# Optimization experiments

Hardware: AMD Instinct MI355X
Metric: run time of the kernel (lower is better)

The kernel has to match this reference:

```python
import jax, jax.numpy as jnp
import numpy as np

D = 160          # SDF grid resolution (D1=D2=D3=D)
LEVEL = 0.0      # marching_cubes(-sdf, level=-0) == level 0 on s = -sdf
N_SMOOTH = 2
LAMBD = 1.0


def _extract_mesh_np():
    """Host-side isosurface extraction (mirrors the module's CPU round-trip).
    Uses marching tetrahedra (6-tet cube decomposition) in place of skimage's
    lewiner marching cubes; topo_correct (undefined in source) is identity.
    Returns (verts [V,3] f32 in normalized coords, faces [F,3] i32, edges [E,2] i32).
    """
    xs = np.arange(D, dtype=np.float32)
    X, Y, Z = np.meshgrid(xs, xs, xs, indexing='ij')
    ctr = (D - 1) / 2.0
    sdf = np.sqrt((X - ctr) ** 2 + (Y - ctr) ** 2 + (Z - ctr) ** 2) - 0.35 * D
    sdf = sdf + 3.0 * np.sin(0.20 * X) * np.sin(0.17 * Y) * np.sin(0.23 * Z)
    s = (-sdf).astype(np.float32)  # extract level-0 isosurface of -sdf
    sflat = s.ravel()
    Ng = D ** 3

    corner_off = [(0, 0, 0), (1, 0, 0), (1, 1, 0), (0, 1, 0),
                  (0, 0, 1), (1, 0, 1), (1, 1, 1), (0, 1, 1)]
    b = np.arange(D - 1)
    BX, BY, BZ = np.meshgrid(b, b, b, indexing='ij')
    BX, BY, BZ = BX.ravel(), BY.ravel(), BZ.ravel()
    gid8 = [((BX + dx) * D + (BY + dy)) * D + (BZ + dz) for dx, dy, dz in corner_off]
    val8 = [sflat[g] for g in gid8]

    TETS = [(0, 5, 1, 6), (0, 1, 2, 6), (0, 2, 3, 6),
            (0, 3, 7, 6), (0, 7, 4, 6), (0, 4, 5, 6)]
    TE = [(0, 1), (0, 2), (0, 3), (1, 2), (1, 3), (2, 3)]  # tet edges
    CASE_TRIS = {1: [(0, 1, 2)], 14: [(0, 1, 2)],
                 2: [(0, 3, 4)], 13: [(0, 3, 4)],
                 4: [(1, 3, 5)], 11: [(1, 3, 5)],
                 8: [(2, 4, 5)], 7: [(2, 4, 5)],
                 3: [(1, 3, 4), (1, 4, 2)], 12: [(1, 3, 4), (1, 4, 2)],
                 5: [(0, 3, 5), (0, 5, 2)], 10: [(0, 3, 5), (0, 5, 2)],
                 6: [(0, 4, 5), (0, 5, 1)], 9: [(0, 4, 5), (0, 5, 1)]}
    bitw = np.array([1, 2, 4, 8])

    tri_keys = []
    for tet in TETS:
        tv = np.stack([val8[c] for c in tet], 1)  # [Nc,4] corner values
        tg = np.stack([gid8[c] for c in tet], 1)  # [Nc,4] corner grid ids
        case = (tv < LEVEL).astype(np.int64) @ bitw
        for c, tris in CASE_TRIS.items():
            sel = np.nonzero(case == c)[0]
            if sel.size == 0:
                continue
            g = tg[sel]
            for tri in tris:
                cols = []
                for e in tri:
                    i, j = TE[e]
                    lo = np.minimum(g[:, i], g[:, j])
                    hi = np.maximum(g[:, i], g[:, j])
                    cols.append(lo * Ng + hi)  # canonical grid-edge key
                tri_keys.append(np.stack(cols, 1))
    tris = np.concatenate(tri_keys, 0)  # [F,3] edge keys
    uk, inv = np.unique(tris, return_inverse=True)
    faces = inv.reshape(-1, 3).astype(np.int32)
    ga = uk // Ng
    gb = uk % Ng
    pa = np.stack(np.unravel_index(ga, (D, D, D)), 1).astype(np.float32)
    pb = np.stack(np.unravel_index(gb, (D, D, D)), 1).astype(np.float32)
    sa = sflat[ga]
    sb = sflat[gb]
    t = ((LEVEL - sa) / (sb - sa)).astype(np.float32)
    verts = pa + t[:, None] * (pb - pa)
    verts = (2.0 * verts - np.float32(D)) / np.float32(D)  # (2v-[D1,D2,D3])/D
    e = np.concatenate([faces[:, [0, 1]], faces[:, [1, 2]], faces[:, [2, 0]]], 0)
    e = np.unique(np.sort(e, 1), axis=0).astype(np.int32)
    return verts.astype(np.float32), faces, e


def setup_inputs() -> dict:
    verts, faces, edges = _extract_mesh_np()
    return {
        'v': jnp.asarray(verts)[None],      # [1,V,3]
        'edges': jnp.asarray(edges),        # [E,2] unique undirected mesh edges
        'faces': jnp.asarray(faces)[None],  # [1,F,3]
    }


def reference(v, edges, faces):
    # Uniform laplacian smoothing: v <- v + lambd * (mean_neighbor(v) - v), x2
    V = v.shape[1]
    src = jnp.concatenate([edges[:, 0], edges[:, 1]])
    dst = jnp.concatenate([edges[:, 1], edges[:, 0]])
    x = v[0]
    deg = jax.ops.segment_sum(jnp.ones(src.shape[0], x.dtype), src, num_segments=V)
    inv_deg = 1.0 / jnp.maximum(deg, 1.0)
    for _ in range(N_SMOOTH):
        nbr = jax.ops.segment_sum(x[dst], src, num_segments=V)
        x = x + LAMBD * (nbr * inv_deg[:, None] - x)
    return x, faces[0]
```

## Files before the change

### kernel.cpp

```cpp
#include <hip/hip_runtime.h>

#define K_ELL 32
#define BS    256

__global__ void build_kernel(const int2* __restrict__ edges, const int* __restrict__ faces,
                             const float* __restrict__ v, float4* __restrict__ v4,
                             int* __restrict__ deg_b, int* __restrict__ offs_a,
                             int* __restrict__ adj_b, float* __restrict__ out_f,
                             int E, int V, int F3) {
    const int tid = blockIdx.x * blockDim.x + threadIdx.x;
    const int T = gridDim.x * blockDim.x;

    for (int i = tid; i <= E; i += T) {
        if (i < E) {
            int2 e = edges[i];
            int r = atomicAdd(&deg_b[e.y], 1);
            if (r < K_ELL) adj_b[(size_t)r * V + e.y] = e.x;
            int lo = (i == 0) ? 0 : edges[i - 1].x + 1;
            for (int a = lo; a <= e.x; a++) offs_a[a] = i;
        } else {
            for (int a = edges[E - 1].x + 1; a <= V; a++) offs_a[a] = E;
        }
    }
    for (int j = tid; j < F3; j += T) out_f[j] = (float)faces[j];
    for (int u = tid; u < V; u += T)
        v4[u] = make_float4(v[3 * u], v[3 * u + 1], v[3 * u + 2], 0.f);
}

template <bool PAD>
__global__ void gather_kernel(const float4* __restrict__ x4, const int2* __restrict__ edges,
                              const int* __restrict__ offs_a, const int* __restrict__ deg_b,
                              const int* __restrict__ adj_b, float* __restrict__ y, int V) {
    int u = blockIdx.x * blockDim.x + threadIdx.x;
    if (u >= V) return;
    int aBeg = offs_a[u], aEnd = offs_a[u + 1];
    int dbFull = deg_b[u];
    int db = dbFull > K_ELL ? K_ELL : dbFull;
    float s0 = 0.f, s1 = 0.f, s2 = 0.f;
    for (int i = aBeg; i < aEnd; i++) {
        float4 p = x4[edges[i].y];
        s0 += p.x; s1 += p.y; s2 += p.z;
    }
    for (int k = 0; k < db; k++) {
        int n = adj_b[(size_t)k * V + u];
        float4 p = x4[n];
        s0 += p.x; s1 += p.y; s2 += p.z;
    }
    int d = (aEnd - aBeg) + dbFull;
    float inv = 1.0f / fmaxf((float)d, 1.0f);
    if (PAD) {
        ((float4*)y)[u] = make_float4(s0 * inv, s1 * inv, s2 * inv, 0.f);
    } else {
        y[3 * u + 0] = s0 * inv;
        y[3 * u + 1] = s1 * inv;
        y[3 * u + 2] = s2 * inv;
    }
}

extern "C" void kernel_launch(void* const* d_in, const int* in_sizes, int n_in,
                              void* d_out, int out_size, void* d_ws, size_t ws_size,
                              hipStream_t stream) {
    const float* v     = (const float*)d_in[0];
    const int2*  edges = (const int2*)d_in[1];
    const int*   faces = (const int*)d_in[2];

    const int V3 = in_sizes[0];
    const int V  = V3 / 3;
    const int E  = in_sizes[1] / 2;
    const int F3 = in_sizes[2];

    float* out_v = (float*)d_out;
    float* out_f = (float*)d_out + V3;

    float4* v4     = (float4*)d_ws;
    float4* x1     = v4 + V;
    int*    adj_b  = (int*)(x1 + V);
    int*    deg_b  = adj_b + (size_t)K_ELL * V;
    int*    offs_a = deg_b + V;

    const int gB = ((F3 > E + 1 ? F3 : E + 1) + BS - 1) / BS;
    const int gV = (V + BS - 1) / BS;

    hipMemsetAsync(deg_b, 0, (size_t)V * sizeof(int), stream);

    build_kernel<<<gB, BS, 0, stream>>>(edges, faces, v, v4, deg_b, offs_a, adj_b,
                                        out_f, E, V, F3);

    gather_kernel<true ><<<gV, BS, 0, stream>>>(v4, edges, offs_a, deg_b, adj_b,
                                                (float*)x1, V);
    gather_kernel<false><<<gV, BS, 0, stream>>>(x1, edges, offs_a, deg_b, adj_b,
                                                out_v, V);
}
```

Before: 99.01 us.

## Build reverse adjacency with LDS-banded atomics instead of global atomics

The reverse-edge adjacency build now uses a count kernel and a fill kernel. Each block owns a vertex range, and destination counts within a nearby band are accumulated with shared-memory atomics. Destinations outside the band go to a global-atomic overflow ELL. The aim is to replace heavy global atomic contention on the degree array with cheap LDS atomics, which works because mesh edges are mostly local. The cost is two extra kernel launches and a larger workspace, and correctness depends on the band assumption plus the K_ELL and K_OVF caps.

```diff
diff --git a/kernel.cpp b/kernel.cpp
--- a/kernel.cpp
+++ b/kernel.cpp
@@ -1,52 +1,114 @@
 #include <hip/hip_runtime.h>
 
 #define K_ELL 32
+#define K_OVF 32
 #define BS    256
+#define TBS   1024
+#define RNG   8192
+#define BAND  8192
+#define RW    (RNG + BAND)
 
-__global__ void build_kernel(const int2* __restrict__ edges, const int* __restrict__ faces,
-                             const float* __restrict__ v, float4* __restrict__ v4,
-                             int* __restrict__ deg_b, int* __restrict__ offs_a,
-                             int* __restrict__ adj_b, float* __restrict__ out_f,
-                             int E, int V, int F3) {
-    const int tid = blockIdx.x * blockDim.x + threadIdx.x;
-    const int T = gridDim.x * blockDim.x;
+__global__ void bound_kernel(const int2* __restrict__ edges, int* __restrict__ offs_a,
+                             int E, int V) {
+    int i = blockIdx.x * blockDim.x + threadIdx.x;
+    if (i < E) {
+        int lo = (i == 0) ? 0 : edges[i - 1].x + 1;
+        int hi = edges[i].x;
+        for (int a = lo; a <= hi; a++) offs_a[a] = i;
+    } else if (i == E) {
+        for (int a = edges[E - 1].x + 1; a <= V; a++) offs_a[a] = E;
+    }
+}
 
-    for (int i = tid; i <= E; i += T) {
-        if (i < E) {
-            int2 e = edges[i];
-            int r = atomicAdd(&deg_b[e.y], 1);
-            if (r < K_ELL) adj_b[(size_t)r * V + e.y] = e.x;
-            int lo = (i == 0) ? 0 : edges[i - 1].x + 1;
-            for (int a = lo; a <= e.x; a++) offs_a[a] = i;
+__global__ __launch_bounds__(TBS) void count_kernel(
+        const int2* __restrict__ edges, const int* __restrict__ offs_a,
+        int* __restrict__ cntN, int* __restrict__ cntF,
+        int* __restrict__ deg_ovf, int* __restrict__ adj_ovf,
+        const int* __restrict__ faces, float* __restrict__ out_f,
+        const float* __restrict__ v, float4* __restrict__ v4,
+        int E, int V, int F3, int NBb) {
+    __shared__ int cnt[RW];
+    if ((int)blockIdx.x >= NBb) {
+        int t = (blockIdx.x - NBb) * TBS + threadIdx.x;
+        int T = (gridDim.x - NBb) * TBS;
+        for (int j = t; j < F3; j += T) out_f[j] = (float)faces[j];
+        for (int u = t; u < V; u += T)
+            v4[u] = make_float4(v[3 * u], v[3 * u + 1], v[3 * u + 2], 0.f);
+        return;
+    }
+    const int v0 = blockIdx.x * RNG;
+    for (int i = threadIdx.x; i < RW; i += TBS) cnt[i] = 0;
+    __syncthreads();
+    const int vEnd = min(v0 + RNG, V);
+    const int eBeg = offs_a[v0], eEnd = offs_a[vEnd];
+    for (int i = eBeg + threadIdx.x; i < eEnd; i += TBS) {
+        int2 e = edges[i];
+        int rel = e.y - (v0 + 1);
+        if (rel < RW) {
+            atomicAdd(&cnt[rel], 1);
         } else {
-            for (int a = edges[E - 1].x + 1; a <= V; a++) offs_a[a] = E;
+            int r = atomicAdd(&deg_ovf[e.y], 1);
+            if (r < K_OVF) adj_ovf[(size_t)r * V + e.y] = e.x;
         }
     }
-    for (int j = tid; j < F3; j += T) out_f[j] = (float)faces[j];
-    for (int u = tid; u < V; u += T)
-        v4[u] = make_float4(v[3 * u], v[3 * u + 1], v[3 * u + 2], 0.f);
+    __syncthreads();
+    for (int i = threadIdx.x; i < RW; i += TBS) {
+        int u = v0 + 1 + i;
+        if (u <= V) {
+            if (i < RNG) cntN[u] = cnt[i];
+            else         cntF[u] = cnt[i];
+        }
+    }
+}
+
+__global__ __launch_bounds__(TBS) void fill_kernel(
+        const int2* __restrict__ edges, const int* __restrict__ offs_a,
+        const int* __restrict__ cntF, int* __restrict__ adj, int V) {
+    __shared__ int cnt[RW];
+    const int v0 = blockIdx.x * RNG;
+    for (int i = threadIdx.x; i < RW; i += TBS) cnt[i] = 0;
+    __syncthreads();
+    const int vEnd = min(v0 + RNG, V);
+    const int eBeg = offs_a[v0], eEnd = offs_a[vEnd];
+    for (int i = eBeg + threadIdx.x; i < eEnd; i += TBS) {
+        int2 e = edges[i];
+        int rel = e.y - (v0 + 1);
+        if (rel < RW) {
+            int r = atomicAdd(&cnt[rel], 1);
+            int slot = (rel < RNG) ? (cntF[e.y] + r) : r;
+            if (slot < K_ELL) adj[(size_t)slot * V + e.y] = e.x;
+        }
+    }
 }
 
 template <bool PAD>
 __global__ void gather_kernel(const float4* __restrict__ x4, const int2* __restrict__ edges,
-                              const int* __restrict__ offs_a, const int* __restrict__ deg_b,
-                              const int* __restrict__ adj_b, float* __restrict__ y, int V) {
+                              const int* __restrict__ offs_a,
+                              const int* __restrict__ cntN, const int* __restrict__ cntF,
+                              const int* __restrict__ deg_ovf,
+                              const int* __restrict__ adj, const int* __restrict__ adj_ovf,
+                              float* __restrict__ y, int V) {
     int u = blockIdx.x * blockDim.x + threadIdx.x;
     if (u >= V) return;
     int aBeg = offs_a[u], aEnd = offs_a[u + 1];
-    int dbFull = deg_b[u];
-    int db = dbFull > K_ELL ? K_ELL : dbFull;
+    int dm  = cntN[u] + cntF[u];
+    int dgo = deg_ovf[u];
     float s0 = 0.f, s1 = 0.f, s2 = 0.f;
     for (int i = aBeg; i < aEnd; i++) {
         float4 p = x4[edges[i].y];
         s0 += p.x; s1 += p.y; s2 += p.z;
     }
-    for (int k = 0; k < db; k++) {
-        int n = adj_b[(size_t)k * V + u];
-        float4 p = x4[n];
+    int dmc = dm > K_ELL ? K_ELL : dm;
+    for (int k = 0; k < dmc; k++) {
+        float4 p = x4[adj[(size_t)k * V + u]];
         s0 += p.x; s1 += p.y; s2 += p.z;
     }
-    int d = (aEnd - aBeg) + dbFull;
+    int doc = dgo > K_OVF ? K_OVF : dgo;
+    for (int k = 0; k < doc; k++) {
+        float4 p = x4[adj_ovf[(size_t)k * V + u]];
+        s0 += p.x; s1 += p.y; s2 += p.z;
+    }
+    int d = (aEnd - aBeg) + dm + dgo;
     float inv = 1.0f / fmaxf((float)d, 1.0f);
     if (PAD) {
         ((float4*)y)[u] = make_float4(s0 * inv, s1 * inv, s2 * inv, 0.f);
@@ -72,22 +134,33 @@
     float* out_v = (float*)d_out;
     float* out_f = (float*)d_out + V3;
 
-    float4* v4     = (float4*)d_ws;
-    float4* x1     = v4 + V;
-    int*    adj_b  = (int*)(x1 + V);
-    int*    deg_b  = adj_b + (size_t)K_ELL * V;
-    int*    offs_a = deg_b + V;
+    float4* v4      = (float4*)d_ws;
+    float4* x1      = v4 + V;
+    int*    adj     = (int*)(x1 + V);
+    int*    adj_ovf = adj + (size_t)K_ELL * V;
+    int*    offs_a  = adj_ovf + (size_t)K_OVF * V;
+    int*    cntN    = offs_a + (V + 1);
+    int*    cntF    = cntN + (V + 1);
+    int*    deg_ovf = cntF + (V + 1);
 
-    const int gB = ((F3 > E + 1 ? F3 : E + 1) + BS - 1) / BS;
+    const int NBb = (V + RNG - 1) / RNG;
+    const int copyElems = F3 > V ? F3 : V;
+    const int NBc = (copyElems + TBS - 1) / TBS;
+    const int gBound = (E + 1 + BS - 1) / BS;
     const int gV = (V + BS - 1) / BS;
 
-    hipMemsetAsync(deg_b, 0, (size_t)V * sizeof(int), stream);
+    hipMemsetAsync(cntN, 0, (size_t)(3 * V + 2) * sizeof(int), stream);
 
-    build_kernel<<<gB, BS, 0, stream>>>(edges, faces, v, v4, deg_b, offs_a, adj_b,
-                                        out_f, E, V, F3);
+    bound_kernel<<<gBound, BS, 0, stream>>>(edges, offs_a, E, V);
 
-    gather_kernel<true ><<<gV, BS, 0, stream>>>(v4, edges, offs_a, deg_b, adj_b,
-                                                (float*)x1, V);
-    gather_kernel<false><<<gV, BS, 0, stream>>>(x1, edges, offs_a, deg_b, adj_b,
-                                                out_v, V);
+    count_kernel<<<NBb + NBc, TBS, 0, stream>>>(edges, offs_a, cntN, cntF,
+                                                deg_ovf, adj_ovf, faces, out_f,
+                                                v, v4, E, V, F3, NBb);
+
+    fill_kernel<<<NBb, TBS, 0, stream>>>(edges, offs_a, cntF, adj, V);
+
+    gather_kernel<true ><<<gV, BS, 0, stream>>>(v4, edges, offs_a, cntN, cntF, deg_ovf,
+                                                adj, adj_ovf, (float*)x1, V);
+    gather_kernel<false><<<gV, BS, 0, stream>>>(x1, edges, offs_a, cntN, cntF, deg_ovf,
+                                                adj, adj_ovf, out_v, V);
 }
```

Result: slower. 121.4 us (+22.6%).
